# Optimization experiments

Hardware: AMD Instinct MI355X
Metric: run time of the kernel (lower is better)

## Reference

```python
import jax, jax.numpy as jnp
import numpy as np

B, S, D, H = 4, 2048, 1024, 16
DK = D // H

def setup_inputs() -> dict:
    key = jax.random.key(0)
    ks = jax.random.split(key, 8)
    scale = 1.0 / np.sqrt(D)
    return {
        "q": jax.random.normal(ks[0], (B, S, D), jnp.float32),
        "k": jax.random.normal(ks[1], (B, S, D), jnp.float32),
        "v": jax.random.normal(ks[2], (B, S, D), jnp.float32),
        "wq": jax.random.normal(ks[3], (D, D), jnp.float32) * scale,
        "bq": jnp.zeros((D,), jnp.float32),
        "wk": jax.random.normal(ks[4], (D, D), jnp.float32) * scale,
        "bk": jnp.zeros((D,), jnp.float32),
        "wv": jax.random.normal(ks[5], (D, D), jnp.float32) * scale,
        "bv": jnp.zeros((D,), jnp.float32),
        "wo": jax.random.normal(ks[6], (D, D), jnp.float32) * scale,
        "bo": jnp.zeros((D,), jnp.float32),
    }

def reference(q, k, v, wq, bq, wk, bk, wv, bv, wo, bo):
    b, s, _ = q.shape
    # projections; split heads -> [b, h, s, d_k]
    def proj(x, w, bias):
        y = x @ w + bias
        return y.reshape(b, -1, H, DK).transpose(0, 2, 1, 3)
    qh, kh, vh = proj(q, wq, bq), proj(k, wk, bk), proj(v, wv, bv)
    scores = jnp.einsum("bhqd,bhkd->bhqk", qh, kh) / np.sqrt(DK).astype(jnp.float32)
    attn = jax.nn.softmax(scores, axis=-1)  # dropout = identity (eval mode)
    out = jnp.einsum("bhqk,bhkd->bhqd", attn, vh)
    out = out.transpose(0, 2, 1, 3).reshape(b, s, D)
    return out @ wo + bo
```

## Files before the change

### kernel.cpp

```cpp
#include <hip/hip_runtime.h>
#include <hip/hip_bf16.h>

#define B_   4
#define S_   2048
#define D_   1024
#define H_   16
#define DK_  64
#define NTOK 8192

typedef __bf16 bf16_t;
typedef __bf16 bf16x8 __attribute__((ext_vector_type(8)));
typedef __bf16 bf16x4 __attribute__((ext_vector_type(4)));
typedef __bf16 bf16x2 __attribute__((ext_vector_type(2)));
typedef float  f32x4  __attribute__((ext_vector_type(4)));
typedef float  f32x16 __attribute__((ext_vector_type(16)));
typedef unsigned u32x4 __attribute__((ext_vector_type(4)));
typedef int    i32x2  __attribute__((ext_vector_type(2)));

__device__ __forceinline__ void gll16(const void* g, void* l) {
  __builtin_amdgcn_global_load_lds(
      (const __attribute__((address_space(1))) void*)g,
      (__attribute__((address_space(3))) void*)l,
      16, 0, 0);
}

__device__ __forceinline__ f32x4 mfma32(bf16x8 a, bf16x8 b, f32x4 c) {
  return __builtin_amdgcn_mfma_f32_16x16x32_bf16(a, b, c, 0, 0, 0);
}

__device__ __forceinline__ f32x16 mfma32x32(bf16x8 a, bf16x8 b, f32x16 c) {
#if defined(__HIP_DEVICE_COMPILE__)
  return __builtin_amdgcn_mfma_f32_32x32x16_bf16(a, b, c, 0, 0, 0);
#else
  (void)a; (void)b;
  return c;
#endif
}

__device__ __forceinline__ float fast_exp2(float x) {
#if defined(__HIP_DEVICE_COMPILE__) && __has_builtin(__builtin_amdgcn_exp2f)
  return __builtin_amdgcn_exp2f(x);
#else
  return exp2f(x);
#endif
}

__device__ __forceinline__ f32x16 zero16() {
  f32x16 z;
#pragma unroll
  for (int i = 0; i < 16; ++i) z[i] = 0.f;
  return z;
}

__device__ __forceinline__ unsigned pkbf(float lo, float hi) {
  bf16x2 t;
  t[0] = (bf16_t)lo;
  t[1] = (bf16_t)hi;
  return __builtin_bit_cast(unsigned, t);
}

__device__ __forceinline__ void plswap(unsigned &x, unsigned &y) {
#if defined(__HIP_DEVICE_COMPILE__)
  i32x2 r = __builtin_amdgcn_permlane32_swap((int)x, (int)y, false, false);
  x = (unsigned)r[0];
  y = (unsigned)r[1];
#endif
}

__device__ __forceinline__ void build_pa(const f32x16 s, bf16x8 &p0, bf16x8 &p1) {
  unsigned A0 = pkbf(fast_exp2(s[0]),  fast_exp2(s[1]));
  unsigned A1 = pkbf(fast_exp2(s[2]),  fast_exp2(s[3]));
  unsigned B0 = pkbf(fast_exp2(s[4]),  fast_exp2(s[5]));
  unsigned B1 = pkbf(fast_exp2(s[6]),  fast_exp2(s[7]));
  unsigned C0 = pkbf(fast_exp2(s[8]),  fast_exp2(s[9]));
  unsigned C1 = pkbf(fast_exp2(s[10]), fast_exp2(s[11]));
  unsigned D0 = pkbf(fast_exp2(s[12]), fast_exp2(s[13]));
  unsigned D1 = pkbf(fast_exp2(s[14]), fast_exp2(s[15]));
  plswap(A0, B0);
  plswap(A1, B1);
  plswap(C0, D0);
  plswap(C1, D1);
  u32x4 lo = {A0, A1, B0, B1};
  u32x4 hi = {C0, C1, D0, D1};
  p0 = __builtin_bit_cast(bf16x8, lo);
  p1 = __builtin_bit_cast(bf16x8, hi);
}

__global__ __launch_bounds__(256) void prep_all(
    const float* __restrict__ q, const float* __restrict__ k,
    const float* __restrict__ v,
    const float* __restrict__ wq, const float* __restrict__ wk,
    const float* __restrict__ wv, const float* __restrict__ wo,
    bf16_t* __restrict__ wtHi, bf16_t* __restrict__ Abf) {
  const int b = blockIdx.x;
  const int t = threadIdx.x;
  __shared__ float T[64][65];

  if (b < 1024) {
    const int z = b >> 8;
    const float* W = (z == 0) ? wq : (z == 1) ? wk : (z == 2) ? wv : wo;
    const int k0 = (b & 15) * 64;
    const int n0 = ((b >> 4) & 15) * 64;
#pragma unroll
    for (int rr = 0; rr < 4; ++rr) {
      int row = rr * 16 + (t >> 4);
      int cc = (t & 15) * 4;
      const float4 vv = *(const float4*)&W[(size_t)(k0 + row) * D_ + n0 + cc];
      T[row][cc + 0] = vv.x; T[row][cc + 1] = vv.y;
      T[row][cc + 2] = vv.z; T[row][cc + 3] = vv.w;
    }
    __syncthreads();
    const int n = t >> 2;
    const int kc = (t & 3) * 16;
    bf16x8 h0, h1;
#pragma unroll
    for (int j = 0; j < 16; ++j) {
      float vv = T[kc + j][n];
      if (j < 8) h0[j] = (bf16_t)vv;
      else       h1[j - 8] = (bf16_t)vv;
    }
    size_t ofs = (size_t)z * 1048576 + (size_t)(n0 + n) * D_ + k0 + kc;
    *(bf16x8*)&wtHi[ofs] = h0; *(bf16x8*)&wtHi[ofs + 8] = h1;
  } else {
    const int bb = b - 1024;
    const int z = bb >> 13;
    const int xb = bb & 8191;
    const float* src = (z == 0) ? q : (z == 1) ? k : v;
    bf16_t* dst = Abf + (size_t)z * 8388608;
    size_t i = ((size_t)xb * 256 + t) * 4;
    float4 x = *(const float4*)&src[i];
    bf16x4 y;
    y[0] = (bf16_t)x.x; y[1] = (bf16_t)x.y;
    y[2] = (bf16_t)x.z; y[3] = (bf16_t)x.w;
    *(bf16x4*)&dst[i] = y;
  }
}

__global__ __launch_bounds__(256) void gemm_qkv_bf16(
    const bf16_t* __restrict__ Abf,
    const float* __restrict__ bq, const float* __restrict__ bk,
    const float* __restrict__ bv,
    const bf16_t* __restrict__ wtHi, bf16_t* __restrict__ outQKV) {
  const int z = blockIdx.z;
  const bf16_t* A   = Abf + (size_t)z * 8388608;
  const float* bias = (z == 0) ? bq : (z == 1) ? bk : bv;
  const bf16_t* WHi = wtHi + (size_t)z * 1048576;
  bf16_t* Out = outQKV + (size_t)z * 8388608;

  const int row0 = blockIdx.x * 128;
  const int col0 = blockIdx.y * 128;
  const int t = threadIdx.x;
  const int w = t >> 6, L = t & 63;
  const int m = L & 15, g = L >> 4;

  __shared__ __align__(16) bf16_t As2[128 * 64];
  __shared__ __align__(16) bf16_t Whi_s[128 * 64];

  f32x4 acc[4][4];
#pragma unroll
  for (int i = 0; i < 4; ++i)
#pragma unroll
    for (int j = 0; j < 4; ++j) acc[i][j] = (f32x4){0.f, 0.f, 0.f, 0.f};

  const int aw0 = (w & 1) * 64;
  const int bw0 = (w >> 1) * 64;

  int srow[4], scol[4];
#pragma unroll
  for (int i = 0; i < 4; ++i) {
    int slot = i * 256 + t;
    srow[i] = slot >> 3;
    scol[i] = (slot & 7) ^ (srow[i] & 7);
  }

  for (int kt = 0; kt < 16; ++kt) {
    const int k0 = kt * 64;
#pragma unroll
    for (int i = 0; i < 4; ++i) {
      gll16(&A[(size_t)(row0 + srow[i]) * D_ + k0 + scol[i] * 8],
            &As2[i * 2048 + w * 512]);
      gll16(&WHi[(size_t)(col0 + srow[i]) * D_ + k0 + scol[i] * 8],
            &Whi_s[i * 2048 + w * 512]);
    }
    __syncthreads();

#pragma unroll
    for (int kh = 0; kh < 2; ++kh) {
      bf16x8 af[4], wh[4];
#pragma unroll
      for (int it = 0; it < 4; ++it) {
        int row = aw0 + it * 16 + m;
        int sl = ((kh * 4 + g) ^ (m & 7)) * 8;
        af[it] = *(const bf16x8*)&As2[row * 64 + sl];
      }
#pragma unroll
      for (int jt = 0; jt < 4; ++jt) {
        int n = bw0 + jt * 16 + m;
        int sl = ((kh * 4 + g) ^ (m & 7)) * 8;
        wh[jt] = *(const bf16x8*)&Whi_s[n * 64 + sl];
      }
#pragma unroll
      for (int it = 0; it < 4; ++it)
#pragma unroll
        for (int jt = 0; jt < 4; ++jt)
          acc[it][jt] = mfma32(af[it], wh[jt], acc[it][jt]);
    }
    __syncthreads();
  }
#pragma unroll
  for (int jt = 0; jt < 4; ++jt) {
    int col = col0 + bw0 + jt * 16 + m;
    float bcol = bias[col];
    int h = col >> 6, d = col & 63;
#pragma unroll
    for (int it = 0; it < 4; ++it) {
      if (z != 2) {
#pragma unroll
        for (int r = 0; r < 4; ++r) {
          int row = row0 + aw0 + it * 16 + g * 4 + r;
          int b = row >> 11, s = row & 2047;
          Out[((size_t)((b * H_ + h) * S_ + s)) * DK_ + d] =
              (bf16_t)(acc[it][jt][r] + bcol);
        }
      } else {
        int row = row0 + aw0 + it * 16 + g * 4;
        int b = row >> 11, s = row & 2047;
        bf16x4 p4;
#pragma unroll
        for (int r = 0; r < 4; ++r) p4[r] = (bf16_t)(acc[it][jt][r] + bcol);
        *(bf16x4*)&Out[((size_t)((b * H_ + h) * DK_ + d)) * S_ + s] = p4;
      }
    }
  }
}

__global__ __launch_bounds__(256) void gemm_qkv_f32(
    const float* __restrict__ Aq, const float* __restrict__ Ak,
    const float* __restrict__ Av,
    const float* __restrict__ bq, const float* __restrict__ bk,
    const float* __restrict__ bv,
    const bf16_t* __restrict__ wtHi, bf16_t* __restrict__ outQKV) {
  const int z = blockIdx.z;
  const float* A    = (z == 0) ? Aq : (z == 1) ? Ak : Av;
  const float* bias = (z == 0) ? bq : (z == 1) ? bk : bv;
  const bf16_t* WHi = wtHi + (size_t)z * 1048576;
  bf16_t* Out = outQKV + (size_t)z * 8388608;

  const int row0 = blockIdx.x * 128;
  const int col0 = blockIdx.y * 128;
  const int t = threadIdx.x;
  const int w = t >> 6, L = t & 63;
  const int m = L & 15, g = L >> 4;

  __shared__ __align__(16) float  As[128 * 32];
  __shared__ __align__(16) bf16_t Whi_s[128 * 32];

  f32x4 acc[4][4];
#pragma unroll
  for (int i = 0; i < 4; ++i)
#pragma unroll
    for (int j = 0; j < 4; ++j) acc[i][j] = (f32x4){0.f, 0.f, 0.f, 0.f};

  const int aw0 = (w & 1) * 64;
  const int bw0 = (w >> 1) * 64;

  for (int kt = 0; kt < 32; ++kt) {
    const int k0 = kt * 32;
#pragma unroll
    for (int rr = 0; rr < 4; ++rr) {
      int lin16 = rr * 256 + t;
      int row = lin16 >> 3;
      int c = (lin16 & 7) ^ (row & 7);
      gll16(&A[(size_t)(row0 + row) * D_ + k0 + c * 4], &As[rr * 1024 + w * 256]);
    }
#pragma unroll
    for (int rr = 0; rr < 2; ++rr) {
      int lin16 = rr * 256 + t;
      int n = lin16 >> 2;
      int c = (lin16 & 3) ^ ((n >> 1) & 3);
      gll16(&WHi[(size_t)(col0 + n) * D_ + k0 + c * 8], &Whi_s[rr * 2048 + w * 512]);
    }
    __syncthreads();

    bf16x8 af[4], wh[4];
#pragma unroll
    for (int it = 0; it < 4; ++it) {
      int row = aw0 + it * 16 + m;
      const f32x4* p = (const f32x4*)&As[row * 32];
      f32x4 x0 = p[(2 * g) ^ (m & 7)];
      f32x4 x1 = p[(2 * g + 1) ^ (m & 7)];
      bf16x8 a;
      a[0] = (bf16_t)x0.x; a[1] = (bf16_t)x0.y; a[2] = (bf16_t)x0.z; a[3] = (bf16_t)x0.w;
      a[4] = (bf16_t)x1.x; a[5] = (bf16_t)x1.y; a[6] = (bf16_t)x1.z; a[7] = (bf16_t)x1.w;
      af[it] = a;
    }
#pragma unroll
    for (int jt = 0; jt < 4; ++jt) {
      int n = bw0 + jt * 16 + m;
      int sl = (g ^ ((m >> 1) & 3)) * 8;
      wh[jt] = *(const bf16x8*)&Whi_s[n * 32 + sl];
    }
#pragma unroll
    for (int it = 0; it < 4; ++it)
#pragma unroll
      for (int jt = 0; jt < 4; ++jt)
        acc[it][jt] = mfma32(af[it], wh[jt], acc[it][jt]);
    __syncthreads();
  }
#pragma unroll
  for (int jt = 0; jt < 4; ++jt) {
    int col = col0 + bw0 + jt * 16 + m;
    float bcol = bias[col];
    int h = col >> 6, d = col & 63;
#pragma unroll
    for (int it = 0; it < 4; ++it) {
      if (z != 2) {
#pragma unroll
        for (int r = 0; r < 4; ++r) {
          int row = row0 + aw0 + it * 16 + g * 4 + r;
          int b = row >> 11, s = row & 2047;
          Out[((size_t)((b * H_ + h) * S_ + s)) * DK_ + d] =
              (bf16_t)(acc[it][jt][r] + bcol);
        }
      } else {
        int row = row0 + aw0 + it * 16 + g * 4;
        int b = row >> 11, s = row & 2047;
        bf16x4 p4;
#pragma unroll
        for (int r = 0; r < 4; ++r) p4[r] = (bf16_t)(acc[it][jt][r] + bcol);
        *(bf16x4*)&Out[((size_t)((b * H_ + h) * DK_ + d)) * S_ + s] = p4;
      }
    }
  }
}

__global__ __launch_bounds__(256, 2) void attn(
    const bf16_t* __restrict__ Qh, const bf16_t* __restrict__ Kh,
    const bf16_t* __restrict__ VhT, bf16_t* __restrict__ Ohi) {
  const int bh = blockIdx.y;
  const int q0 = blockIdx.x * 128;
  const int t = threadIdx.x, w = t >> 6;
  const int lane = t & 63;
  const int lo5 = lane & 31, hi = lane >> 5;

  __shared__ __align__(16) bf16_t Ks[64 * 64];
  __shared__ __align__(16) bf16_t Vt[64 * 64];

  const size_t qbase = (size_t)bh * S_ * DK_;
  const size_t vbase = (size_t)bh * DK_ * S_;

  const int qrow = q0 + w * 32 + lo5;
  bf16x8 qf[4];
#pragma unroll
  for (int ks = 0; ks < 4; ++ks) {
    bf16x8 v = *(const bf16x8*)&Qh[qbase + (size_t)qrow * DK_ + ks * 16 + hi * 8];
#pragma unroll
    for (int j = 0; j < 8; ++j) v[j] = (bf16_t)(0.18033688f * (float)v[j]);
    qf[ks] = v;
  }

  bf16x8 ones;
#pragma unroll
  for (int j = 0; j < 8; ++j) ones[j] = (bf16_t)1.f;

  int offs[4];
#pragma unroll
  for (int ks = 0; ks < 4; ++ks)
    offs[ks] = lo5 * 64 + (((ks * 2 + hi) ^ (lo5 & 7)) * 8);

  f32x16 oacc0 = zero16(), oacc1 = zero16(), lacc = zero16();

  for (int kv0 = 0; kv0 < S_; kv0 += 64) {
#pragma unroll
    for (int rr = 0; rr < 2; ++rr) {
      int lin16 = rr * 256 + t;
      int rrow = lin16 >> 3;
      int c = (lin16 & 7) ^ (rrow & 7);
      gll16(&Kh[qbase + (size_t)(kv0 + rrow) * DK_ + c * 8], &Ks[rr * 2048 + w * 512]);
      gll16(&VhT[vbase + (size_t)rrow * S_ + kv0 + c * 8], &Vt[rr * 2048 + w * 512]);
    }
    __syncthreads();

    f32x16 sc0 = zero16(), sc1 = zero16();
#pragma unroll
    for (int ks = 0; ks < 4; ++ks) {
      bf16x8 k0 = *(const bf16x8*)&Ks[offs[ks]];
      bf16x8 k1 = *(const bf16x8*)&Ks[offs[ks] + 2048];
      sc0 = mfma32x32(k0, qf[ks], sc0);
      sc1 = mfma32x32(k1, qf[ks], sc1);
    }

    bf16x8 pa0, pa1, pa2, pa3;
    build_pa(sc0, pa0, pa1);
    build_pa(sc1, pa2, pa3);

#pragma unroll
    for (int ks = 0; ks < 4; ++ks) {
      bf16x8 pb = (ks == 0) ? pa0 : (ks == 1) ? pa1 : (ks == 2) ? pa2 : pa3;
      lacc = mfma32x32(ones, pb, lacc);
      bf16x8 v0 = *(const bf16x8*)&Vt[offs[ks]];
      bf16x8 v1 = *(const bf16x8*)&Vt[offs[ks] + 2048];
      oacc0 = mfma32x32(v0, pb, oacc0);
      oacc1 = mfma32x32(v1, pb, oacc1);
    }
    __syncthreads();
  }

  const int b = bh >> 4, h = bh & 15;
  const float inv = 1.f / lacc[0];
  const size_t rowofs = ((size_t)(b * S_ + qrow)) * D_ + h * DK_;
#pragma unroll
  for (int rg = 0; rg < 4; ++rg) {
    bf16x4 o0, o1;
#pragma unroll
    for (int j = 0; j < 4; ++j) {
      o0[j] = (bf16_t)(oacc0[rg * 4 + j] * inv);
      o1[j] = (bf16_t)(oacc1[rg * 4 + j] * inv);
    }
    *(bf16x4*)&Ohi[rowofs + rg * 8 + hi * 4] = o0;
    *(bf16x4*)&Ohi[rowofs + 32 + rg * 8 + hi * 4] = o1;
  }
}

__global__ __launch_bounds__(256) void gemm_out(
    const bf16_t* __restrict__ Ahi, const bf16_t* __restrict__ wtHi,
    const float* __restrict__ bias, float* __restrict__ Out) {
  const bf16_t* WHi = wtHi + (size_t)3 * 1048576;
  const int row0 = blockIdx.x * 128;
  const int col0 = blockIdx.y * 128;
  const int t = threadIdx.x;
  const int w = t >> 6, L = t & 63;
  const int m = L & 15, g = L >> 4;

  __shared__ __align__(16) bf16_t Ahi_s[2][128 * 64];
  __shared__ __align__(16) bf16_t Whi_s[2][128 * 64];

  f32x4 acc[4][4];
#pragma unroll
  for (int i = 0; i < 4; ++i)
#pragma unroll
    for (int j = 0; j < 4; ++j) acc[i][j] = (f32x4){0.f, 0.f, 0.f, 0.f};

  const int aw0 = (w & 1) * 64;
  const int bw0 = (w >> 1) * 64;

  int srow[4], scol[4];
#pragma unroll
  for (int i = 0; i < 4; ++i) {
    int slot = i * 256 + t;
    srow[i] = slot >> 3;
    scol[i] = (slot & 7) ^ (srow[i] & 7);
  }

#define OSTAGE(buf, k0)                                                        \
  do {                                                                         \
    _Pragma("unroll")                                                          \
    for (int i = 0; i < 4; ++i) {                                              \
      gll16(&Ahi[(size_t)(row0 + srow[i]) * D_ + (k0) + scol[i] * 8],          \
            &Ahi_s[buf][i * 2048 + w * 512]);                                  \
      gll16(&WHi[(size_t)(col0 + srow[i]) * D_ + (k0) + scol[i] * 8],          \
            &Whi_s[buf][i * 2048 + w * 512]);                                  \
    }                                                                          \
  } while (0)

  OSTAGE(0, 0);
  __syncthreads();

  for (int kt = 0; kt < 16; ++kt) {
    const int c = kt & 1;
    if (kt < 15) OSTAGE(c ^ 1, (kt + 1) * 64);

    const bf16_t* as_b = &Ahi_s[c][0];
    const bf16_t* ws_b = &Whi_s[c][0];
#pragma unroll
    for (int kh = 0; kh < 2; ++kh) {
      bf16x8 ah[4], wh[4];
#pragma unroll
      for (int it = 0; it < 4; ++it) {
        int row = aw0 + it * 16 + m;
        int sl = ((kh * 4 + g) ^ (m & 7)) * 8;
        ah[it] = *(const bf16x8*)&as_b[row * 64 + sl];
      }
#pragma unroll
      for (int jt = 0; jt < 4; ++jt) {
        int n = bw0 + jt * 16 + m;
        int sl = ((kh * 4 + g) ^ (m & 7)) * 8;
        wh[jt] = *(const bf16x8*)&ws_b[n * 64 + sl];
      }
#pragma unroll
      for (int it = 0; it < 4; ++it)
#pragma unroll
        for (int jt = 0; jt < 4; ++jt)
          acc[it][jt] = mfma32(ah[it], wh[jt], acc[it][jt]);
    }
    __syncthreads();
  }
#undef OSTAGE

#pragma unroll
  for (int jt = 0; jt < 4; ++jt) {
    int col = col0 + bw0 + jt * 16 + m;
    float bcol = bias[col];
#pragma unroll
    for (int it = 0; it < 4; ++it)
#pragma unroll
      for (int r = 0; r < 4; ++r) {
        int row = row0 + aw0 + it * 16 + g * 4 + r;
        Out[(size_t)row * D_ + col] = acc[it][jt][r] + bcol;
      }
  }
}

extern "C" void kernel_launch(void* const* d_in, const int* in_sizes, int n_in,
                              void* d_out, int out_size, void* d_ws, size_t ws_size,
                              hipStream_t stream) {
  const float* q  = (const float*)d_in[0];
  const float* k  = (const float*)d_in[1];
  const float* v  = (const float*)d_in[2];
  const float* wq = (const float*)d_in[3];
  const float* bq = (const float*)d_in[4];
  const float* wk = (const float*)d_in[5];
  const float* bk = (const float*)d_in[6];
  const float* wv = (const float*)d_in[7];
  const float* bv = (const float*)d_in[8];
  const float* wo = (const float*)d_in[9];
  const float* bo = (const float*)d_in[10];
  float* out = (float*)d_out;

  char* ws = (char*)d_ws;
  bf16_t* wtHi = (bf16_t*)(ws);
  bf16_t* QKVh = (bf16_t*)(ws + (8ull << 20));
  bf16_t* Ohi  = (bf16_t*)(ws + (56ull << 20));
  bf16_t* Abf  = (bf16_t*)(ws + (56ull << 20));

  const bool big = ws_size >= (104ull << 20);

  if (big) {
    hipLaunchKernelGGL(prep_all, dim3(25600), dim3(256), 0, stream,
                       q, k, v, wq, wk, wv, wo, wtHi, Abf);
    hipLaunchKernelGGL(gemm_qkv_bf16, dim3(64, 8, 3), dim3(256), 0, stream,
                       Abf, bq, bk, bv, wtHi, QKVh);
  } else {
    hipLaunchKernelGGL(prep_all, dim3(1024), dim3(256), 0, stream,
                       q, k, v, wq, wk, wv, wo, wtHi, (bf16_t*)wtHi );
    hipLaunchKernelGGL(gemm_qkv_f32, dim3(64, 8, 3), dim3(256), 0, stream,
                       q, k, v, bq, bk, bv, wtHi, QKVh);
  }
  hipLaunchKernelGGL(attn, dim3(16, 64), dim3(256), 0, stream,
                     QKVh, QKVh + 8388608, QKVh + 16777216, Ohi);
  hipLaunchKernelGGL(gemm_out, dim3(64, 8), dim3(256), 0, stream,
                     Ohi, wtHi, bo, out);
}
```

Baseline: 339.7 us.

## Double-buffer QKV GEMM with partial vmcnt waits and XCD-aware block swizzle

The bf16 QKV projection GEMM now uses two shared-memory buffers with a K-tile of 32, prefetching the next tile while computing the current one. Both GEMMs replace __syncthreads with an explicit vmcnt wait plus s_barrier, so only the older loads must finish before compute. Both also flatten the grid to 1D and remap block ids so that blocks landing on the same XCD share A/W tiles, aiming for better L2 reuse. The hand-set vmcnt counts depend on the exact number of outstanding loads, which is fragile if the code generator reorders them.

```diff
diff --git a/kernel.cpp b/kernel.cpp
--- a/kernel.cpp
+++ b/kernel.cpp
@@ -141,20 +141,24 @@
     const float* __restrict__ bq, const float* __restrict__ bk,
     const float* __restrict__ bv,
     const bf16_t* __restrict__ wtHi, bf16_t* __restrict__ outQKV) {
-  const int z = blockIdx.z;
+  const int d = blockIdx.x;
+  const int swz = (d >> 9) * 512 + (d & 7) * 64 + ((d & 511) >> 3);
+  const int z = swz >> 9;
+  const int rblk = swz & 511;
+  const int row0 = (rblk >> 3) * 128;
+  const int col0 = (rblk & 7) * 128;
+
   const bf16_t* A   = Abf + (size_t)z * 8388608;
   const float* bias = (z == 0) ? bq : (z == 1) ? bk : bv;
   const bf16_t* WHi = wtHi + (size_t)z * 1048576;
   bf16_t* Out = outQKV + (size_t)z * 8388608;
 
-  const int row0 = blockIdx.x * 128;
-  const int col0 = blockIdx.y * 128;
   const int t = threadIdx.x;
   const int w = t >> 6, L = t & 63;
   const int m = L & 15, g = L >> 4;
 
-  __shared__ __align__(16) bf16_t As2[128 * 64];
-  __shared__ __align__(16) bf16_t Whi_s[128 * 64];
+  __shared__ __align__(16) bf16_t As2[2][128 * 32];
+  __shared__ __align__(16) bf16_t Whi_s[2][128 * 32];
 
   f32x4 acc[4][4];
 #pragma unroll
@@ -165,53 +169,67 @@
   const int aw0 = (w & 1) * 64;
   const int bw0 = (w >> 1) * 64;
 
-  int srow[4], scol[4];
-#pragma unroll
-  for (int i = 0; i < 4; ++i) {
-    int slot = i * 256 + t;
-    srow[i] = slot >> 3;
-    scol[i] = (slot & 7) ^ (srow[i] & 7);
-  }
-
-  for (int kt = 0; kt < 16; ++kt) {
-    const int k0 = kt * 64;
-#pragma unroll
-    for (int i = 0; i < 4; ++i) {
-      gll16(&A[(size_t)(row0 + srow[i]) * D_ + k0 + scol[i] * 8],
-            &As2[i * 2048 + w * 512]);
-      gll16(&WHi[(size_t)(col0 + srow[i]) * D_ + k0 + scol[i] * 8],
-            &Whi_s[i * 2048 + w * 512]);
-    }
-    __syncthreads();
-
-#pragma unroll
-    for (int kh = 0; kh < 2; ++kh) {
-      bf16x8 af[4], wh[4];
-#pragma unroll
-      for (int it = 0; it < 4; ++it) {
-        int row = aw0 + it * 16 + m;
-        int sl = ((kh * 4 + g) ^ (m & 7)) * 8;
-        af[it] = *(const bf16x8*)&As2[row * 64 + sl];
-      }
-#pragma unroll
-      for (int jt = 0; jt < 4; ++jt) {
-        int n = bw0 + jt * 16 + m;
-        int sl = ((kh * 4 + g) ^ (m & 7)) * 8;
-        wh[jt] = *(const bf16x8*)&Whi_s[n * 64 + sl];
-      }
-#pragma unroll
-      for (int it = 0; it < 4; ++it)
-#pragma unroll
-        for (int jt = 0; jt < 4; ++jt)
-          acc[it][jt] = mfma32(af[it], wh[jt], acc[it][jt]);
-    }
-    __syncthreads();
-  }
+  int n_[2], c_[2];
+#pragma unroll
+  for (int rr = 0; rr < 2; ++rr) {
+    int lin16 = rr * 256 + t;
+    n_[rr] = lin16 >> 2;
+    c_[rr] = (lin16 & 3) ^ ((n_[rr] >> 1) & 3);
+  }
+
+#define QSTAGE(buf, k0)                                                        \
+  do {                                                                         \
+    _Pragma("unroll")                                                          \
+    for (int rr = 0; rr < 2; ++rr) {                                           \
+      gll16(&A[(size_t)(row0 + n_[rr]) * D_ + (k0) + c_[rr] * 8],              \
+            &As2[buf][rr * 2048 + w * 512]);                                   \
+      gll16(&WHi[(size_t)(col0 + n_[rr]) * D_ + (k0) + c_[rr] * 8],            \
+            &Whi_s[buf][rr * 2048 + w * 512]);                                 \
+    }                                                                          \
+  } while (0)
+
+  QSTAGE(0, 0);
+
+  for (int kt = 0; kt < 32; ++kt) {
+    const int c = kt & 1;
+    if (kt < 31) {
+      QSTAGE(c ^ 1, (kt + 1) * 32);
+      asm volatile("s_waitcnt vmcnt(4)" ::: "memory");
+    } else {
+      asm volatile("s_waitcnt vmcnt(0)" ::: "memory");
+    }
+    __builtin_amdgcn_s_barrier();
+
+    const bf16_t* as_b = &As2[c][0];
+    const bf16_t* ws_b = &Whi_s[c][0];
+    bf16x8 af[4], wh[4];
+#pragma unroll
+    for (int it = 0; it < 4; ++it) {
+      int row = aw0 + it * 16 + m;
+      int sl = (g ^ ((m >> 1) & 3)) * 8;
+      af[it] = *(const bf16x8*)&as_b[row * 32 + sl];
+    }
+#pragma unroll
+    for (int jt = 0; jt < 4; ++jt) {
+      int n = bw0 + jt * 16 + m;
+      int sl = (g ^ ((m >> 1) & 3)) * 8;
+      wh[jt] = *(const bf16x8*)&ws_b[n * 32 + sl];
+    }
+#pragma unroll
+    for (int it = 0; it < 4; ++it)
+#pragma unroll
+      for (int jt = 0; jt < 4; ++jt)
+        acc[it][jt] = mfma32(af[it], wh[jt], acc[it][jt]);
+
+    __builtin_amdgcn_s_barrier();
+  }
+#undef QSTAGE
+
 #pragma unroll
   for (int jt = 0; jt < 4; ++jt) {
     int col = col0 + bw0 + jt * 16 + m;
     float bcol = bias[col];
-    int h = col >> 6, d = col & 63;
+    int h = col >> 6, dd = col & 63;
 #pragma unroll
     for (int it = 0; it < 4; ++it) {
       if (z != 2) {
@@ -219,7 +237,7 @@
         for (int r = 0; r < 4; ++r) {
           int row = row0 + aw0 + it * 16 + g * 4 + r;
           int b = row >> 11, s = row & 2047;
-          Out[((size_t)((b * H_ + h) * S_ + s)) * DK_ + d] =
+          Out[((size_t)((b * H_ + h) * S_ + s)) * DK_ + dd] =
               (bf16_t)(acc[it][jt][r] + bcol);
         }
       } else {
@@ -228,7 +246,7 @@
         bf16x4 p4;
 #pragma unroll
         for (int r = 0; r < 4; ++r) p4[r] = (bf16_t)(acc[it][jt][r] + bcol);
-        *(bf16x4*)&Out[((size_t)((b * H_ + h) * DK_ + d)) * S_ + s] = p4;
+        *(bf16x4*)&Out[((size_t)((b * H_ + h) * DK_ + dd)) * S_ + s] = p4;
       }
     }
   }
@@ -311,7 +329,7 @@
   for (int jt = 0; jt < 4; ++jt) {
     int col = col0 + bw0 + jt * 16 + m;
     float bcol = bias[col];
-    int h = col >> 6, d = col & 63;
+    int h = col >> 6, dd = col & 63;
 #pragma unroll
     for (int it = 0; it < 4; ++it) {
       if (z != 2) {
@@ -319,7 +337,7 @@
         for (int r = 0; r < 4; ++r) {
           int row = row0 + aw0 + it * 16 + g * 4 + r;
           int b = row >> 11, s = row & 2047;
-          Out[((size_t)((b * H_ + h) * S_ + s)) * DK_ + d] =
+          Out[((size_t)((b * H_ + h) * S_ + s)) * DK_ + dd] =
               (bf16_t)(acc[it][jt][r] + bcol);
         }
       } else {
@@ -328,7 +346,7 @@
         bf16x4 p4;
 #pragma unroll
         for (int r = 0; r < 4; ++r) p4[r] = (bf16_t)(acc[it][jt][r] + bcol);
-        *(bf16x4*)&Out[((size_t)((b * H_ + h) * DK_ + d)) * S_ + s] = p4;
+        *(bf16x4*)&Out[((size_t)((b * H_ + h) * DK_ + dd)) * S_ + s] = p4;
       }
     }
   }
@@ -426,8 +444,11 @@
     const bf16_t* __restrict__ Ahi, const bf16_t* __restrict__ wtHi,
     const float* __restrict__ bias, float* __restrict__ Out) {
   const bf16_t* WHi = wtHi + (size_t)3 * 1048576;
-  const int row0 = blockIdx.x * 128;
-  const int col0 = blockIdx.y * 128;
+  const int d = blockIdx.x;
+  const int swz = (d & 7) * 64 + (d >> 3);
+  const int row0 = (swz >> 3) * 128;
+  const int col0 = (swz & 7) * 128;
+
   const int t = threadIdx.x;
   const int w = t >> 6, L = t & 63;
   const int m = L & 15, g = L >> 4;
@@ -464,11 +485,16 @@
   } while (0)
 
   OSTAGE(0, 0);
-  __syncthreads();
 
   for (int kt = 0; kt < 16; ++kt) {
     const int c = kt & 1;
-    if (kt < 15) OSTAGE(c ^ 1, (kt + 1) * 64);
+    if (kt < 15) {
+      OSTAGE(c ^ 1, (kt + 1) * 64);
+      asm volatile("s_waitcnt vmcnt(8)" ::: "memory");
+    } else {
+      asm volatile("s_waitcnt vmcnt(0)" ::: "memory");
+    }
+    __builtin_amdgcn_s_barrier();
 
     const bf16_t* as_b = &Ahi_s[c][0];
     const bf16_t* ws_b = &Whi_s[c][0];
@@ -493,7 +519,7 @@
         for (int jt = 0; jt < 4; ++jt)
           acc[it][jt] = mfma32(ah[it], wh[jt], acc[it][jt]);
     }
-    __syncthreads();
+    __builtin_amdgcn_s_barrier();
   }
 #undef OSTAGE
 
@@ -538,7 +564,7 @@
   if (big) {
     hipLaunchKernelGGL(prep_all, dim3(25600), dim3(256), 0, stream,
                        q, k, v, wq, wk, wv, wo, wtHi, Abf);
-    hipLaunchKernelGGL(gemm_qkv_bf16, dim3(64, 8, 3), dim3(256), 0, stream,
+    hipLaunchKernelGGL(gemm_qkv_bf16, dim3(1536), dim3(256), 0, stream,
                        Abf, bq, bk, bv, wtHi, QKVh);
   } else {
     hipLaunchKernelGGL(prep_all, dim3(1024), dim3(256), 0, stream,
@@ -548,6 +574,6 @@
   }
   hipLaunchKernelGGL(attn, dim3(16, 64), dim3(256), 0, stream,
                      QKVh, QKVh + 8388608, QKVh + 16777216, Ohi);
-  hipLaunchKernelGGL(gemm_out, dim3(64, 8), dim3(256), 0, stream,
+  hipLaunchKernelGGL(gemm_out, dim3(512), dim3(256), 0, stream,
                      Ohi, wtHi, bo, out);
 }
```

Result: no change. 336.0 us (-1.1%).
